# Kernel tuning notes

Measured on AMD Instinct MI355X. Metric: run time of the kernel, lower is better.

Reference implementation:

```python
import jax, jax.numpy as jnp
import numpy as np

B, S, E = 2, 2048, 1024
H = 16
D = E // H  # head_dim = 64
SCALE = D ** -0.5


def _rope_cos_sin(seq_len, dim, dtype=jnp.float32):
    inv_freq = 1.0 / (10000.0 ** (jnp.arange(0, dim, 2, dtype=jnp.float32) / dim))
    pos = jnp.arange(seq_len, dtype=jnp.float32)
    freqs = pos[:, None] * inv_freq[None, :]  # [S, D/2]
    return jnp.cos(freqs).astype(dtype), jnp.sin(freqs).astype(dtype)


def _apply_rope(x, cos, sin):
    # x: [B, H, S, D]; interleaved complex rotation on (even, odd) pairs
    x2 = x.reshape(*x.shape[:-1], D // 2, 2)
    xr, xi = x2[..., 0], x2[..., 1]
    c = cos[None, None, :, :]
    s = sin[None, None, :, :]
    out_r = xr * c - xi * s
    out_i = xr * s + xi * c
    return jnp.stack([out_r, out_i], axis=-1).reshape(x.shape)


def setup_inputs() -> dict:
    key = jax.random.key(0)
    k1, k2, k3, k4, k5 = jax.random.split(key, 5)
    query = jax.random.normal(k1, (B, S, E), dtype=jnp.float32)
    key_t = jax.random.normal(k2, (B, S, E), dtype=jnp.float32)
    value = jax.random.normal(k3, (B, S, E), dtype=jnp.float32)
    w_qkv = jax.random.normal(k4, (3 * E, E), dtype=jnp.float32) * 0.02
    w_out = jax.random.normal(k5, (E, E), dtype=jnp.float32) * 0.02
    return {"query": query, "key": key_t, "value": value,
            "w_qkv": w_qkv, "w_out": w_out}


def reference(query, key, value, w_qkv, w_out):
    # Fused QKV projection from query only (matches original module)
    qkv = jnp.einsum('bse,fe->bsf', query, w_qkv)  # [B, S, 3E]
    q, k, v = jnp.split(qkv, 3, axis=-1)
    to_heads = lambda t: t.reshape(B, S, H, D).transpose(0, 2, 1, 3)  # [B,H,S,D]
    q, k, v = to_heads(q), to_heads(k), to_heads(v)

    cos, sin = _rope_cos_sin(S, D, q.dtype)
    q = _apply_rope(q, cos, sin)
    k = _apply_rope(k, cos, sin)

    # Standard scaled dot-product attention (eval mode, no mask, no dropout)
    attn = jnp.einsum('bhsd,bhtd->bhst', q, k) * SCALE
    attn = jax.nn.softmax(attn.astype(jnp.float32), axis=-1).astype(q.dtype)
    ctx = jnp.einsum('bhst,bhtd->bhsd', attn, v)  # [B,H,S,D]

    out = ctx.transpose(0, 2, 1, 3).reshape(B, S, E)
    return jnp.einsum('bse,fe->bsf', out, w_out)
```

## Files before the change

### kernel.cpp

```cpp
#include <hip/hip_runtime.h>
#include <math.h>

typedef __attribute__((ext_vector_type(8))) __bf16 bf16x8;
typedef __attribute__((ext_vector_type(4))) __bf16 bf16x4;
typedef __attribute__((ext_vector_type(4))) float f32x4;

constexpr int kBATCH = 2;
constexpr int kS = 2048;
constexpr int kE = 1024;
constexpr int kH = 16;
constexpr int kD = 64;
constexpr float kScale = 0.125f;
constexpr float kQScale = 0.125f * 1.44269504088896340736f;

__device__ inline void gl2lds16(const void* g, void* l) {
    __builtin_amdgcn_global_load_lds((const __attribute__((address_space(1))) void*)g,
                                     (__attribute__((address_space(3))) void*)l, 16, 0, 0);
}

__global__ __launch_bounds__(256) void cvt2_kernel(const float* __restrict__ a, __bf16* __restrict__ oa, int na,
                                                   const float* __restrict__ b, __bf16* __restrict__ ob) {
    int idx = (blockIdx.x * 256 + threadIdx.x) * 4;
    const float* src;
    __bf16* dst;
    if (idx < na) { src = a + idx; dst = oa + idx; }
    else          { src = b + (idx - na); dst = ob + (idx - na); }
    float4 f = *(const float4*)src;
    bf16x4 r;
    r[0] = (__bf16)f.x; r[1] = (__bf16)f.y; r[2] = (__bf16)f.z; r[3] = (__bf16)f.w;
    *(bf16x4*)dst = r;
}

template <int TN, typename TC>
__global__ __launch_bounds__(256) void gemm_bt_kernel(const __bf16* __restrict__ A,
                                                      const __bf16* __restrict__ W,
                                                      TC* __restrict__ C,
                                                      int M, int N, int K) {
    constexpr int NI = TN / 32;
    __shared__ __bf16 As[128 * 64] __attribute__((aligned(16)));
    __shared__ __bf16 Bs[TN * 64] __attribute__((aligned(16)));

    const int tid  = threadIdx.x;
    const int lane = tid & 63;
    const int quad = lane >> 4;
    const int l16  = lane & 15;
    const int rx   = l16 & 7;
    const int wave = tid >> 6;
    const int wm   = (wave >> 1) * 64;
    const int wn   = (wave & 1) * (TN / 2);
    const int m0   = blockIdx.y * 128;
    const int n0   = blockIdx.x * TN;

    const int srow8  = lane >> 3;
    const int schunk = ((lane & 7) ^ srow8) * 8;

    f32x4 zero = {0.f, 0.f, 0.f, 0.f};
    f32x4 acc[4][NI];
#pragma unroll
    for (int i = 0; i < 4; ++i)
#pragma unroll
        for (int j = 0; j < NI; ++j) acc[i][j] = zero;

    for (int kt = 0; kt < K; kt += 64) {
        __syncthreads();
#pragma unroll
        for (int i = 0; i < 4; ++i) {
            int rbase = wave * 32 + i * 8;
            gl2lds16(A + (size_t)(m0 + rbase + srow8) * K + kt + schunk, &As[rbase * 64]);
        }
#pragma unroll
        for (int i = 0; i < NI; ++i) {
            int rbase = wave * (TN / 4) + i * 8;
            gl2lds16(W + (size_t)(n0 + rbase + srow8) * K + kt + schunk, &Bs[rbase * 64]);
        }
        __syncthreads();

#pragma unroll
        for (int kk = 0; kk < 2; ++kk) {
            bf16x8 af[4], bf[NI];
#pragma unroll
            for (int mi = 0; mi < 4; ++mi)
                af[mi] = *(const bf16x8*)(&As[(wm + mi * 16 + l16) * 64 + (((kk * 4 + quad) ^ rx)) * 8]);
#pragma unroll
            for (int ni = 0; ni < NI; ++ni)
                bf[ni] = *(const bf16x8*)(&Bs[(wn + ni * 16 + l16) * 64 + (((kk * 4 + quad) ^ rx)) * 8]);
#pragma unroll
            for (int mi = 0; mi < 4; ++mi)
#pragma unroll
                for (int ni = 0; ni < NI; ++ni)
                    acc[mi][ni] = __builtin_amdgcn_mfma_f32_16x16x32_bf16(af[mi], bf[ni], acc[mi][ni], 0, 0, 0);
        }
    }

#pragma unroll
    for (int mi = 0; mi < 4; ++mi)
#pragma unroll
        for (int ni = 0; ni < NI; ++ni)
#pragma unroll
            for (int r = 0; r < 4; ++r) {
                int row = m0 + wm + mi * 16 + quad * 4 + r;
                int col = n0 + wn + ni * 16 + l16;
                C[(size_t)row * N + col] = (TC)acc[mi][ni][r];
            }
}

__global__ __launch_bounds__(256) void rope_vtrans_kernel(const __bf16* __restrict__ qkv,
                                                          __bf16* __restrict__ qd,
                                                          __bf16* __restrict__ kd,
                                                          __bf16* __restrict__ vt) {
    __shared__ __bf16 tile[64 * 72] __attribute__((aligned(16)));

    if (blockIdx.x < 8192) {
        int tid = blockIdx.x * 256 + threadIdx.x;
        int i = tid & 31;
        int h = (tid >> 5) & (kH - 1);
        int s = (tid >> 9) & (kS - 1);
        int b = tid >> 20;

        size_t rowbase = (size_t)(b * kS + s) * (3 * kE);
        int coff = h * kD + 2 * i;

        float qr = (float)qkv[rowbase + coff];
        float qi = (float)qkv[rowbase + coff + 1];
        float kr = (float)qkv[rowbase + kE + coff];
        float ki = (float)qkv[rowbase + kE + coff + 1];

        float inv = expf(-(float)i * (9.210340371976184f / 32.0f));
        float ang = (float)s * inv;
        float cv = cosf(ang);
        float sv = sinf(ang);

        size_t qbase = ((size_t)(b * kH + h) * kS + s) * kD + 2 * i;
        qd[qbase]     = (__bf16)(kQScale * (qr * cv - qi * sv));
        qd[qbase + 1] = (__bf16)(kQScale * (qr * sv + qi * cv));
        kd[qbase]     = (__bf16)(kr * cv - ki * sv);
        kd[qbase + 1] = (__bf16)(kr * sv + ki * cv);
    } else {
        int flat = blockIdx.x - 8192;
        int s0 = (flat & 31) * 64;
        int bh = flat >> 5;
        int b = bh >> 4, h = bh & 15;
        int tid = threadIdx.x;

#pragma unroll
        for (int p = 0; p < 2; ++p) {
            int c = tid + p * 256;
            int r = c >> 3, jc = c & 7;
            *(bf16x8*)&tile[r * 72 + jc * 8] =
                *(const bf16x8*)(qkv + (size_t)(b * kS + s0 + r) * (3 * kE) + 2 * kE + h * kD + jc * 8);
        }
        __syncthreads();
#pragma unroll
        for (int p = 0; p < 2; ++p) {
            int c = tid + p * 256;
            int d = c >> 3, jt = c & 7;
            bf16x8 v;
#pragma unroll
            for (int u = 0; u < 8; ++u) {
                int src = (jt >> 2) * 32 + ((u >> 2) << 4) + ((jt & 3) << 2) + (u & 3);
                v[u] = tile[src * 72 + d];
            }
            *(bf16x8*)(vt + (size_t)(bh * kD + d) * kS + s0 + jt * 8) = v;
        }
    }
}

__global__ __launch_bounds__(256, 2) void attn_kernel(const __bf16* __restrict__ qd,
                                                      const __bf16* __restrict__ kd,
                                                      const __bf16* __restrict__ vt,
                                                      __bf16* __restrict__ ctx,
                                                      const float* __restrict__ wout,
                                                      __bf16* __restrict__ woutb) {
    __shared__ __bf16 Ks[2][64 * 64] __attribute__((aligned(16)));
    __shared__ __bf16 Vs[2][64 * 64] __attribute__((aligned(16)));

    const int lane = threadIdx.x & 63;
    const int wave = threadIdx.x >> 6;
    const int quad = lane >> 4;
    const int l16  = lane & 15;
    const int rx   = l16 & 7;

    {
        int base = blockIdx.x * 2048 + threadIdx.x * 8;
#pragma unroll
        for (int p = 0; p < 2; ++p) {
            float4 f = *(const float4*)(wout + base + p * 4);
            bf16x4 r;
            r[0] = (__bf16)f.x; r[1] = (__bf16)f.y; r[2] = (__bf16)f.z; r[3] = (__bf16)f.w;
            *(bf16x4*)(woutb + base + p * 4) = r;
        }
    }

    const int flat = blockIdx.x;
    const int s    = flat >> 3;
    const int bh   = (flat & 7) * 4 + (s >> 4);
    const int q0   = (s & 15) * 128;
    const int b  = bh >> 4;
    const int h  = bh & 15;

    const __bf16* qp = qd + (size_t)bh * kS * kD;
    const __bf16* kp = kd + (size_t)bh * kS * kD;
    const __bf16* vp = vt + (size_t)bh * kD * kS;

    const int srow8  = lane >> 3;
    const int schunk = ((lane & 7) ^ srow8) * 8;

    bf16x8 aq[2][2];
#pragma unroll
    for (int qg = 0; qg < 2; ++qg) {
        const __bf16* qrow = qp + (size_t)(q0 + wave * 32 + qg * 16 + l16) * kD + quad * 8;
        aq[qg][0] = *(const bf16x8*)(qrow);
        aq[qg][1] = *(const bf16x8*)(qrow + 32);
    }

    bf16x8 vone;
#pragma unroll
    for (int u = 0; u < 8; ++u) vone[u] = (__bf16)1.0f;

    f32x4 zero = {0.f, 0.f, 0.f, 0.f};
    f32x4 acc[2][4];
    f32x4 asum[2] = {zero, zero};
#pragma unroll
    for (int qg = 0; qg < 2; ++qg)
#pragma unroll
        for (int i = 0; i < 4; ++i) acc[qg][i] = zero;

    int koff[4][2], voff[4][2];
#pragma unroll
    for (int g = 0; g < 4; ++g) {
        int row = g * 16 + l16;
        koff[g][0] = row * 64 + ((quad       ^ rx)) * 8;
        koff[g][1] = row * 64 + (((quad + 4) ^ rx)) * 8;
        voff[g][0] = row * 64 + ((quad       ^ (row & 7))) * 8;
        voff[g][1] = row * 64 + (((quad + 4) ^ (row & 7))) * 8;
    }

    const __bf16* kst[2];
    const __bf16* vst[2];
#pragma unroll
    for (int c = 0; c < 2; ++c) {
        int i = wave * 2 + c;
        kst[c] = kp + (size_t)(i * 8 + srow8) * kD + schunk;
        vst[c] = vp + (size_t)(i * 8 + srow8) * kS + schunk;
    }

#pragma unroll
    for (int c = 0; c < 2; ++c) {
        gl2lds16(kst[c], &Ks[0][(wave * 2 + c) * 512]);
        gl2lds16(vst[c], &Vs[0][(wave * 2 + c) * 512]);
        kst[c] += 64 * kD;
        vst[c] += 64;
    }

    const int nT = kS / 64;

    auto body = [&](int buf, bool prefetch) __attribute__((always_inline)) -> void {
        __syncthreads();
        if (prefetch) {
#pragma unroll
            for (int c = 0; c < 2; ++c) {
                gl2lds16(kst[c], &Ks[buf ^ 1][(wave * 2 + c) * 512]);
                gl2lds16(vst[c], &Vs[buf ^ 1][(wave * 2 + c) * 512]);
                kst[c] += 64 * kD;
                vst[c] += 64;
            }
        }

        f32x4 sg[2][4];
        __builtin_amdgcn_s_setprio(1);
#pragma unroll
        for (int g = 0; g < 4; ++g) {
            bf16x8 a0 = *(const bf16x8*)&Ks[buf][koff[g][0]];
            bf16x8 a1 = *(const bf16x8*)&Ks[buf][koff[g][1]];
#pragma unroll
            for (int qg = 0; qg < 2; ++qg) {
                f32x4 t = __builtin_amdgcn_mfma_f32_16x16x32_bf16(a0, aq[qg][0], zero, 0, 0, 0);
                sg[qg][g] = __builtin_amdgcn_mfma_f32_16x16x32_bf16(a1, aq[qg][1], t, 0, 0, 0);
            }
        }
        __builtin_amdgcn_s_setprio(0);

        bf16x8 ap[2][2];
#pragma unroll
        for (int qg = 0; qg < 2; ++qg)
#pragma unroll
            for (int r = 0; r < 4; ++r) {
                ap[qg][0][r]     = (__bf16)__builtin_amdgcn_exp2f(sg[qg][0][r]);
                ap[qg][0][4 + r] = (__bf16)__builtin_amdgcn_exp2f(sg[qg][1][r]);
                ap[qg][1][r]     = (__bf16)__builtin_amdgcn_exp2f(sg[qg][2][r]);
                ap[qg][1][4 + r] = (__bf16)__builtin_amdgcn_exp2f(sg[qg][3][r]);
            }

        __builtin_amdgcn_s_setprio(1);
#pragma unroll
        for (int qg = 0; qg < 2; ++qg) {
            asum[qg] = __builtin_amdgcn_mfma_f32_16x16x32_bf16(ap[qg][0], vone, asum[qg], 0, 0, 0);
            asum[qg] = __builtin_amdgcn_mfma_f32_16x16x32_bf16(ap[qg][1], vone, asum[qg], 0, 0, 0);
        }

#pragma unroll
        for (int nt = 0; nt < 4; ++nt) {
            bf16x8 bv0 = *(const bf16x8*)&Vs[buf][voff[nt][0]];
            bf16x8 bv1 = *(const bf16x8*)&Vs[buf][voff[nt][1]];
#pragma unroll
            for (int qg = 0; qg < 2; ++qg) {
                acc[qg][nt] = __builtin_amdgcn_mfma_f32_16x16x32_bf16(ap[qg][0], bv0, acc[qg][nt], 0, 0, 0);
                acc[qg][nt] = __builtin_amdgcn_mfma_f32_16x16x32_bf16(ap[qg][1], bv1, acc[qg][nt], 0, 0, 0);
            }
        }
        __builtin_amdgcn_s_setprio(0);
    };

    for (int it = 0; it < nT; it += 2) {
        body(0, true);
        body(1, it + 2 < nT);
    }

#pragma unroll
    for (int qg = 0; qg < 2; ++qg)
#pragma unroll
        for (int r = 0; r < 4; ++r) {
            float inv_l = 1.0f / asum[qg][r];
            int srow_q = q0 + wave * 32 + qg * 16 + quad * 4 + r;
#pragma unroll
            for (int nt = 0; nt < 4; ++nt) {
                int col = h * kD + nt * 16 + l16;
                ctx[(size_t)(b * kS + srow_q) * kE + col] = (__bf16)(acc[qg][nt][r] * inv_l);
            }
        }
}

extern "C" void kernel_launch(void* const* d_in, const int* in_sizes, int n_in,
                              void* d_out, int out_size, void* d_ws, size_t ws_size,
                              hipStream_t stream) {
    const float* query = (const float*)d_in[0];
    const float* w_qkv = (const float*)d_in[3];
    const float* w_out = (const float*)d_in[4];
    float* out = (float*)d_out;

    const int M = kBATCH * kS;
    const int nQ = M * kE;
    const int nWqkv = 3 * kE * kE;

    char* ws = (char*)d_ws;
    __bf16* qkv_raw = (__bf16*)ws;
    __bf16* ctx     = (__bf16*)ws;
    __bf16* w_out_b = (__bf16*)(ws + (size_t)8388608);
    __bf16* qd      = (__bf16*)(ws + (size_t)25165824);
    __bf16* kd      = (__bf16*)(ws + (size_t)33554432);
    __bf16* vt      = (__bf16*)(ws + (size_t)41943040);
    __bf16* query_b = qd;
    __bf16* w_qkv_b = kd;

    cvt2_kernel<<<(nQ + nWqkv) / 1024, 256, 0, stream>>>(query, query_b, nQ, w_qkv, w_qkv_b);

    gemm_bt_kernel<128, __bf16>
        <<<dim3(3 * kE / 128, M / 128), 256, 0, stream>>>(query_b, w_qkv_b, qkv_raw, M, 3 * kE, kE);

    rope_vtrans_kernel<<<8192 + 1024, 256, 0, stream>>>(qkv_raw, qd, kd, vt);

    attn_kernel<<<512, 256, 0, stream>>>(qd, kd, vt, ctx, w_out, w_out_b);

    gemm_bt_kernel<64, float>
        <<<dim3(kE / 64, M / 128), 256, 0, stream>>>(ctx, w_out_b, out, M, kE, kE);
}
```

Baseline: 200.0 us.

## Software-pipeline attention: overlap next tile QK^T with current exp and PV

```diff
diff --git a/kernel.cpp b/kernel.cpp
--- a/kernel.cpp
+++ b/kernel.cpp
@@ -172,7 +172,7 @@
                                                       const float* __restrict__ wout,
                                                       __bf16* __restrict__ woutb) {
     __shared__ __bf16 Ks[2][64 * 64] __attribute__((aligned(16)));
-    __shared__ __bf16 Vs[2][64 * 64] __attribute__((aligned(16)));
+    __shared__ __bf16 Vs[4][64 * 64] __attribute__((aligned(16)));
 
     const int lane = threadIdx.x & 63;
     const int wave = threadIdx.x >> 6;
@@ -225,6 +225,8 @@
 #pragma unroll
         for (int i = 0; i < 4; ++i) acc[qg][i] = zero;
 
+    f32x4 sgb[2][2][4];
+
     int koff[4][2], voff[4][2];
 #pragma unroll
     for (int g = 0; g < 4; ++g) {
@@ -244,76 +246,93 @@
         vst[c] = vp + (size_t)(i * 8 + srow8) * kS + schunk;
     }
 
-#pragma unroll
-    for (int c = 0; c < 2; ++c) {
-        gl2lds16(kst[c], &Ks[0][(wave * 2 + c) * 512]);
-        gl2lds16(vst[c], &Vs[0][(wave * 2 + c) * 512]);
-        kst[c] += 64 * kD;
-        vst[c] += 64;
-    }
-
-    const int nT = kS / 64;
-
-    auto body = [&](int buf, bool prefetch) __attribute__((always_inline)) -> void {
-        __syncthreads();
-        if (prefetch) {
-#pragma unroll
-            for (int c = 0; c < 2; ++c) {
-                gl2lds16(kst[c], &Ks[buf ^ 1][(wave * 2 + c) * 512]);
-                gl2lds16(vst[c], &Vs[buf ^ 1][(wave * 2 + c) * 512]);
-                kst[c] += 64 * kD;
-                vst[c] += 64;
-            }
-        }
-
-        f32x4 sg[2][4];
-        __builtin_amdgcn_s_setprio(1);
+    auto stage = [&](int ks, int vs) __attribute__((always_inline)) -> void {
+#pragma unroll
+        for (int c = 0; c < 2; ++c) {
+            gl2lds16(kst[c], &Ks[ks][(wave * 2 + c) * 512]);
+            gl2lds16(vst[c], &Vs[vs][(wave * 2 + c) * 512]);
+            kst[c] += 64 * kD;
+            vst[c] += 64;
+        }
+    };
+
+    auto qk = [&](int kbuf, int par) __attribute__((always_inline)) -> void {
 #pragma unroll
         for (int g = 0; g < 4; ++g) {
-            bf16x8 a0 = *(const bf16x8*)&Ks[buf][koff[g][0]];
-            bf16x8 a1 = *(const bf16x8*)&Ks[buf][koff[g][1]];
+            bf16x8 a0 = *(const bf16x8*)&Ks[kbuf][koff[g][0]];
+            bf16x8 a1 = *(const bf16x8*)&Ks[kbuf][koff[g][1]];
 #pragma unroll
             for (int qg = 0; qg < 2; ++qg) {
                 f32x4 t = __builtin_amdgcn_mfma_f32_16x16x32_bf16(a0, aq[qg][0], zero, 0, 0, 0);
-                sg[qg][g] = __builtin_amdgcn_mfma_f32_16x16x32_bf16(a1, aq[qg][1], t, 0, 0, 0);
-            }
-        }
-        __builtin_amdgcn_s_setprio(0);
-
-        bf16x8 ap[2][2];
+                sgb[par][qg][g] = __builtin_amdgcn_mfma_f32_16x16x32_bf16(a1, aq[qg][1], t, 0, 0, 0);
+            }
+        }
+    };
+
+    auto expand = [&](bf16x8 (&ap)[2][2], int par) __attribute__((always_inline)) -> void {
 #pragma unroll
         for (int qg = 0; qg < 2; ++qg)
 #pragma unroll
             for (int r = 0; r < 4; ++r) {
-                ap[qg][0][r]     = (__bf16)__builtin_amdgcn_exp2f(sg[qg][0][r]);
-                ap[qg][0][4 + r] = (__bf16)__builtin_amdgcn_exp2f(sg[qg][1][r]);
-                ap[qg][1][r]     = (__bf16)__builtin_amdgcn_exp2f(sg[qg][2][r]);
-                ap[qg][1][4 + r] = (__bf16)__builtin_amdgcn_exp2f(sg[qg][3][r]);
-            }
-
-        __builtin_amdgcn_s_setprio(1);
+                ap[qg][0][r]     = (__bf16)__builtin_amdgcn_exp2f(sgb[par][qg][0][r]);
+                ap[qg][0][4 + r] = (__bf16)__builtin_amdgcn_exp2f(sgb[par][qg][1][r]);
+                ap[qg][1][r]     = (__bf16)__builtin_amdgcn_exp2f(sgb[par][qg][2][r]);
+                ap[qg][1][4 + r] = (__bf16)__builtin_amdgcn_exp2f(sgb[par][qg][3][r]);
+            }
+    };
+
+    auto sumpv = [&](int vbuf, bf16x8 (&ap)[2][2]) __attribute__((always_inline)) -> void {
 #pragma unroll
         for (int qg = 0; qg < 2; ++qg) {
             asum[qg] = __builtin_amdgcn_mfma_f32_16x16x32_bf16(ap[qg][0], vone, asum[qg], 0, 0, 0);
             asum[qg] = __builtin_amdgcn_mfma_f32_16x16x32_bf16(ap[qg][1], vone, asum[qg], 0, 0, 0);
         }
-
 #pragma unroll
         for (int nt = 0; nt < 4; ++nt) {
-            bf16x8 bv0 = *(const bf16x8*)&Vs[buf][voff[nt][0]];
-            bf16x8 bv1 = *(const bf16x8*)&Vs[buf][voff[nt][1]];
+            bf16x8 bv0 = *(const bf16x8*)&Vs[vbuf][voff[nt][0]];
+            bf16x8 bv1 = *(const bf16x8*)&Vs[vbuf][voff[nt][1]];
 #pragma unroll
             for (int qg = 0; qg < 2; ++qg) {
                 acc[qg][nt] = __builtin_amdgcn_mfma_f32_16x16x32_bf16(ap[qg][0], bv0, acc[qg][nt], 0, 0, 0);
                 acc[qg][nt] = __builtin_amdgcn_mfma_f32_16x16x32_bf16(ap[qg][1], bv1, acc[qg][nt], 0, 0, 0);
             }
         }
+    };
+
+    auto body = [&](int kbuf, int vprev, int vnext, bool pf, int pin)
+        __attribute__((always_inline)) -> void {
+        __syncthreads();
+        if (pf) stage(kbuf ^ 1, vnext);
+        bf16x8 ap[2][2];
+        expand(ap, pin);
+        __builtin_amdgcn_s_setprio(1);
+        qk(kbuf, pin ^ 1);
+        sumpv(vprev, ap);
         __builtin_amdgcn_s_setprio(0);
     };
 
-    for (int it = 0; it < nT; it += 2) {
-        body(0, true);
-        body(1, it + 2 < nT);
+    stage(0, 0);
+    __syncthreads();
+    stage(1, 1);
+    __builtin_amdgcn_s_setprio(1);
+    qk(0, 0);
+    __builtin_amdgcn_s_setprio(0);
+
+#pragma unroll 1
+    for (int t0 = 1; t0 < 29; t0 += 4) {
+        body(1, 0, 2, true, 0);
+        body(0, 1, 3, true, 1);
+        body(1, 2, 0, true, 0);
+        body(0, 3, 1, true, 1);
+    }
+    body(1, 0, 2, true, 0);
+    body(0, 1, 3, true, 1);
+    body(1, 2, 0, false, 0);
+
+    {
+        bf16x8 ap[2][2];
+        expand(ap, 1);
+        sumpv(3, ap);
     }
 
 #pragma unroll
```

New measurement: 197.2 us. About the same (-1.4%).
